# Performance work log

Measured on AMD Instinct MI355X. Metric: run time of the kernel, lower is better.

Reference implementation:

```python
import jax, jax.numpy as jnp
import numpy as np
from jax import lax

MEM = 100          # forced by head_h.view(2, 100)
IN_DIM = 300
N_SENT = 512
N_WORD = 64
VOCAB = 128000
N_HEAD = 8
D = 2 * MEM        # 200
WINDOWS = (1, 2, 3, 4, 5, 6, 7)
NF = 10


def setup_inputs() -> dict:
    key = jax.random.key(0)
    ks = jax.random.split(key, 32)
    def rn(i, shp, s=0.05):
        return jax.random.normal(ks[i], shp, jnp.float32) * s
    inp = dict(
        head_tokens=jax.random.randint(ks[0], (N_WORD,), 1, VOCAB),
        body_tokens=jax.random.randint(ks[1], (N_SENT, N_WORD), 1, VOCAB),
        emb=rn(2, (VOCAB, IN_DIM)),
        wih_f=rn(3, (4 * MEM, IN_DIM)), whh_f=rn(4, (4 * MEM, MEM)),
        bih_f=rn(5, (4 * MEM,)), bhh_f=rn(6, (4 * MEM,)),
        wih_b=rn(7, (4 * MEM, IN_DIM)), whh_b=rn(8, (4 * MEM, MEM)),
        bih_b=rn(9, (4 * MEM,)), bhh_b=rn(10, (4 * MEM,)),
        wq=rn(11, (N_HEAD, D, D)), bq=rn(12, (N_HEAD, D)),
        wk=rn(13, (N_HEAD, D, D)), bk=rn(14, (N_HEAD, D)),
        wv=rn(15, (N_HEAD, D, D)), bv=rn(16, (N_HEAD, D)),
        concat_w=rn(17, (D, N_HEAD * D)), concat_b=rn(18, (D,)),
        feat_w=rn(19, (D, N_SENT * D)), feat_b=rn(20, (D,)),
        conv_b=rn(21, (len(WINDOWS), NF)),
    )
    for j, w in enumerate(WINDOWS):
        inp['conv_w%d' % w] = rn(22 + j, (NF, 1, w, D))
    return inp


def _lstm_dir(x, wih, whh, bih, bhh):
    # x: [T, IN_DIM] -> final hidden [MEM]; torch gate order i, f, g, o
    def step(carry, xt):
        h, c = carry
        g = xt @ wih.T + h @ whh.T + bih + bhh
        i, f, gg, o = jnp.split(g, 4)
        c = jax.nn.sigmoid(f) * c + jax.nn.sigmoid(i) * jnp.tanh(gg)
        h = jax.nn.sigmoid(o) * jnp.tanh(c)
        return (h, c), None
    z = jnp.zeros((MEM,), x.dtype)
    (h, _), _ = lax.scan(step, (z, z), x)
    return h


def _bilstm(x, p):
    wih_f, whh_f, bih_f, bhh_f, wih_b, whh_b, bih_b, bhh_b = p
    hf = _lstm_dir(x, wih_f, whh_f, bih_f, bhh_f)
    hb = _lstm_dir(x[::-1], wih_b, whh_b, bih_b, bhh_b)
    return jnp.concatenate([hf, hb])  # [D]


def _forward(head_tokens, body_tokens, emb, lstm_p, wq, bq, wk, bk, wv, bv,
             concat_w, concat_b, feat_w, feat_b, conv_ws, conv_b):
    # headline encoder
    Bi_Head_h = _bilstm(emb[head_tokens], lstm_p)          # [D]
    # per-sentence BiLSTM over the whole (padded) doc, batched via vmap
    body_x = emb[body_tokens]                              # [S, W, IN_DIM]
    sent_enc = jax.vmap(lambda x: _bilstm(x, lstm_p))(body_x)  # [S, D]
    # 8 single-head self-attentions (indicator == 1 path)
    Q = jnp.einsum('sd,hed->hse', sent_enc, wq) + bq[:, None, :]
    K = jnp.einsum('sd,hed->hse', sent_enc, wk) + bk[:, None, :]
    V = jnp.einsum('sd,hed->hse', sent_enc, wv) + bv[:, None, :]
    sim = jnp.einsum('hse,hte->hst', Q, K) / jnp.sqrt(jnp.float32(D))
    attn = jax.nn.softmax(sim, axis=1)   # torch softmax(dim=0) over [S, S]
    out = jnp.einsum('hst,hte->hse', attn, V)              # [H, S, D]
    head_concat = jnp.transpose(out, (1, 0, 2)).reshape(N_SENT, N_HEAD * D)
    multi = head_concat @ concat_w.T + concat_b            # [S, D]
    high_sent_feature = feat_w @ multi.reshape(-1) + feat_b  # [D]
    # TextCNN over sentence encodings
    x4 = sent_enc[None, None]                              # [1, 1, S, D]
    pooled = []
    for j, (w, cw) in enumerate(zip(WINDOWS, conv_ws)):
        y = lax.conv_general_dilated(
            x4, cw, (1, 1), [(w - 1, w - 1), (0, 0)],
            dimension_numbers=('NCHW', 'OIHW', 'NCHW'))    # [1, NF, S+w-1, 1]
        pooled.append(jnp.max(y[0, :, :, 0], axis=1) + conv_b[j])  # [NF]
    high_sim_pooled = jnp.stack(pooled)                    # [7, NF]
    return high_sent_feature, Bi_Head_h, high_sim_pooled


def reference(head_tokens, body_tokens, emb,
              wih_f, whh_f, bih_f, bhh_f, wih_b, whh_b, bih_b, bhh_b,
              wq, bq, wk, bk, wv, bv, concat_w, concat_b, feat_w, feat_b,
              conv_w1, conv_w2, conv_w3, conv_w4, conv_w5, conv_w6, conv_w7,
              conv_b):
    lstm_p = (wih_f, whh_f, bih_f, bhh_f, wih_b, whh_b, bih_b, bhh_b)
    conv_ws = (conv_w1, conv_w2, conv_w3, conv_w4, conv_w5, conv_w6, conv_w7)
    return _forward(head_tokens, body_tokens, emb, lstm_p, wq, bq, wk, bk,
                    wv, bv, concat_w, concat_b, feat_w, feat_b, conv_ws, conv_b)
```

## Files before the change

kernel.cpp:

```cpp
#include <hip/hip_runtime.h>

typedef _Float16 half8 __attribute__((ext_vector_type(8)));

__device__ __forceinline__ unsigned short f2bf(float f) {
  unsigned u = __float_as_uint(f);
  u += 0x7FFFu + ((u >> 16) & 1u);
  return (unsigned short)(u >> 16);
}
__device__ __forceinline__ float bf2f(unsigned short b) {
  return __uint_as_float(((unsigned)b) << 16);
}
__device__ __forceinline__ float sigf(float x) {
  return __builtin_amdgcn_rcpf(1.f + __expf(-x));
}
__device__ __forceinline__ float tanhf_(float x) {
  float t = __expf(2.f * x);
  return 1.f - 2.f * __builtin_amdgcn_rcpf(t + 1.f);
}

#define NROWS 32832

__global__ __launch_bounds__(256)
void k0_cw4(const float* __restrict__ cw, float* __restrict__ cw4) {
  int idx = blockIdx.x * 256 + threadIdx.x;
  if (idx < 320000) {
    int d = idx / 1600, k = idx % 1600;
    cw4[(size_t)(k >> 2) * 800 + d * 4 + (k & 3)] = cw[idx];
  }
}

__global__ __launch_bounds__(128)
void k1_proj(const int* __restrict__ head_toks, const int* __restrict__ body_toks,
             const float* __restrict__ emb,
             const float* __restrict__ wihf, const float* __restrict__ wihb,
             const float* __restrict__ bihf, const float* __restrict__ bhhf,
             const float* __restrict__ bihb, const float* __restrict__ bhhb,
             unsigned short* __restrict__ XP) {
  __shared__ float At[32][132];
  __shared__ float Wt[32][132];
  __shared__ int toks[128];
  const int tid = threadIdx.x;
  const int r0 = blockIdx.x * 128;
  const int c0 = blockIdx.y * 128;
  if (tid < 128) {
    int r = r0 + tid;
    int tok = 0;
    if (r < NROWS) {
      int u = r >> 6, t = r & 63;
      tok = (u < 512) ? body_toks[u * 64 + t] : head_toks[t];
    }
    toks[tid] = tok;
  }
  const int ty = tid >> 3;
  const int tx = tid & 7;
  float acc[8][16];
#pragma unroll
  for (int i = 0; i < 8; ++i)
#pragma unroll
    for (int j = 0; j < 16; ++j) acc[i][j] = 0.f;

  for (int k0 = 0; k0 < 300; k0 += 32) {
    __syncthreads();
#pragma unroll
    for (int it = 0; it < 8; ++it) {
      int slot = tid + it * 128;
      int rr = slot >> 3, kq = slot & 7;
      int k = k0 + kq * 4;
      float4 v = make_float4(0.f, 0.f, 0.f, 0.f);
      if (k < 300) v = *(const float4*)(emb + (size_t)toks[rr] * 300 + k);
      At[kq * 4 + 0][rr] = v.x; At[kq * 4 + 1][rr] = v.y;
      At[kq * 4 + 2][rr] = v.z; At[kq * 4 + 3][rr] = v.w;
    }
#pragma unroll
    for (int it = 0; it < 8; ++it) {
      int slot = tid + it * 128;
      int cc = slot >> 3, kq = slot & 7;
      int gc = c0 + cc;
      int k = k0 + kq * 4;
      float4 v = make_float4(0.f, 0.f, 0.f, 0.f);
      if (k < 300 && gc < 800) {
        const float* wp = (gc < 400) ? (wihf + (size_t)gc * 300)
                                     : (wihb + (size_t)(gc - 400) * 300);
        v = *(const float4*)(wp + k);
      }
      Wt[kq * 4 + 0][cc] = v.x; Wt[kq * 4 + 1][cc] = v.y;
      Wt[kq * 4 + 2][cc] = v.z; Wt[kq * 4 + 3][cc] = v.w;
    }
    __syncthreads();
#pragma unroll 4
    for (int k = 0; k < 32; ++k) {
      float a[8], b[16];
      *(float4*)&a[0] = *(const float4*)&At[k][ty * 8];
      *(float4*)&a[4] = *(const float4*)&At[k][ty * 8 + 4];
#pragma unroll
      for (int q = 0; q < 4; ++q)
        *(float4*)&b[q * 4] = *(const float4*)&Wt[k][tx * 4 + q * 32];
#pragma unroll
      for (int i = 0; i < 8; ++i)
#pragma unroll
        for (int j = 0; j < 16; ++j)
          acc[i][j] = fmaf(a[i], b[j], acc[i][j]);
    }
  }
  float biasv[16];
#pragma unroll
  for (int j = 0; j < 16; ++j) {
    int gc = c0 + tx * 4 + (j >> 2) * 32 + (j & 3);
    float bv = 0.f;
    if (gc < 400) bv = bihf[gc] + bhhf[gc];
    else if (gc < 800) bv = bihb[gc - 400] + bhhb[gc - 400];
    biasv[j] = bv;
  }
#pragma unroll
  for (int i = 0; i < 8; ++i) {
    int r = r0 + ty * 8 + i;
    if (r >= NROWS) continue;
#pragma unroll
    for (int q = 0; q < 4; ++q) {
      int colq = c0 + tx * 4 + q * 32;
      if (colq >= 800) continue;
      ushort4 pk;
      pk.x = f2bf(acc[i][q * 4 + 0] + biasv[q * 4 + 0]);
      pk.y = f2bf(acc[i][q * 4 + 1] + biasv[q * 4 + 1]);
      pk.z = f2bf(acc[i][q * 4 + 2] + biasv[q * 4 + 2]);
      pk.w = f2bf(acc[i][q * 4 + 3] + biasv[q * 4 + 3]);
      *(ushort4*)(XP + (size_t)r * 800 + colq) = pk;
    }
  }
}

#define K2_W2_SLOTS (4 * 2 * 13 * 64)
#define K2_LDS_BYTES (K2_W2_SLOTS * 16 + 5 * 104 * 4)

__global__ __launch_bounds__(320)
void k2_lstm(const unsigned short* __restrict__ XP,
             const float* __restrict__ whhf, const float* __restrict__ whhb,
             float* __restrict__ sentRM, float* __restrict__ sentT,
             float* __restrict__ dout) {
  extern __shared__ char smem[];
  _Float16* W2 = (_Float16*)smem;
  float* hall = (float*)(smem + K2_W2_SLOTS * 16);
  const int tid = threadIdx.x;
  const int wave = tid >> 6;
  const int lane = tid & 63;
  const int wg = blockIdx.x;
  const bool fwd = wg < 128;
  const int wg2 = fwd ? wg : wg - 128;
  const float* whh = fwd ? whhf : whhb;

  for (int idx = tid; idx < K2_W2_SLOTS; idx += 320) {
    int lane_s = idx & 63;
    int kb = (idx >> 6) % 13;
    int gm = idx / (13 * 64);
    int m = (gm & 1) * 64 + lane_s;
    int g = gm >> 1;
    half8 hv;
#pragma unroll
    for (int i = 0; i < 8; ++i) {
      int k = kb * 8 + i;
      float v = 0.f;
      if (m < 100 && k < 100) v = whh[(size_t)(g * 100 + m) * 100 + k];
      hv[i] = (_Float16)v;
    }
    *(half8*)(W2 + (size_t)idx * 8) = hv;
  }

  int u;
  if (wave < 4) u = wg2 * 4 + wave;
  else u = (wg2 == 0) ? 512 : -1;

  float* hme = hall + wave * 104;
  if (u >= 0) {
    for (int i = lane; i < 104; i += 64) hme[i] = 0.f;
  }
  __syncthreads();
  if (u < 0) return;

  const int off = fwd ? 0 : 400;
  const int doff = fwd ? 0 : 100;
  const int ubase = u * 64;
  const int mm0 = lane;
  const bool v1 = (64 + lane) < 100;
  const int mm1 = v1 ? 64 + lane : 0;

  unsigned short xp[4][2];
  {
    int r = ubase + (fwd ? 0 : 63);
    const unsigned short* rp = XP + (size_t)r * 800 + off;
#pragma unroll
    for (int g = 0; g < 4; ++g) { xp[g][0] = rp[g * 100 + mm0]; xp[g][1] = rp[g * 100 + mm1]; }
  }
  float c0 = 0.f, c1 = 0.f, hl0 = 0.f, hl1 = 0.f;

  for (int t = 0; t < 64; ++t) {
    float acc[4][2];
#pragma unroll
    for (int g = 0; g < 4; ++g) { acc[g][0] = bf2f(xp[g][0]); acc[g][1] = bf2f(xp[g][1]); }
    {
      int tn = (t + 1 < 64) ? t + 1 : 63;
      int r = ubase + (fwd ? tn : 63 - tn);
      const unsigned short* rp = XP + (size_t)r * 800 + off;
#pragma unroll
      for (int g = 0; g < 4; ++g) { xp[g][0] = rp[g * 100 + mm0]; xp[g][1] = rp[g * 100 + mm1]; }
    }
#pragma unroll
    for (int kb = 0; kb < 13; ++kb) {
      float hv[8];
      *(float4*)&hv[0] = *(const float4*)(hme + kb * 8);
      *(float4*)&hv[4] = *(const float4*)(hme + kb * 8 + 4);
#pragma unroll
      for (int g = 0; g < 4; ++g)
#pragma unroll
        for (int ms = 0; ms < 2; ++ms) {
          half8 w = *(const half8*)(W2 + ((size_t)((g * 2 + ms) * 13 + kb) * 64 + lane) * 8);
          float a = acc[g][ms];
#pragma unroll
          for (int i = 0; i < 8; ++i) a = fmaf((float)w[i], hv[i], a);
          acc[g][ms] = a;
        }
    }
    {
      float si = sigf(acc[0][0]), sf = sigf(acc[1][0]), so = sigf(acc[3][0]);
      float tg = tanhf_(acc[2][0]);
      c0 = sf * c0 + si * tg;
      hl0 = so * tanhf_(c0);
      hme[mm0] = hl0;
    }
    if (v1) {
      float si = sigf(acc[0][1]), sf = sigf(acc[1][1]), so = sigf(acc[3][1]);
      float tg = tanhf_(acc[2][1]);
      c1 = sf * c1 + si * tg;
      hl1 = so * tanhf_(c1);
      hme[64 + lane] = hl1;
    }
  }
  {
    int d = doff + mm0;
    sentRM[(size_t)u * 200 + d] = hl0;
    sentT[(size_t)d * 520 + u] = hl0;
    if (u == 512) dout[200 + d] = hl0;
  }
  if (v1) {
    int d = doff + 64 + lane;
    sentRM[(size_t)u * 200 + d] = hl1;
    sentT[(size_t)d * 520 + u] = hl1;
    if (u == 512) dout[200 + d] = hl1;
  }
}

__global__ __launch_bounds__(256)
void k3_qkv(const float* __restrict__ sentT,
            const float* __restrict__ wq, const float* __restrict__ bq,
            const float* __restrict__ wk, const float* __restrict__ bk,
            const float* __restrict__ wv, const float* __restrict__ bv,
            float* __restrict__ QT, float* __restrict__ KT, float* __restrict__ V) {
  __shared__ float slds[32 * 64];
  __shared__ float wt[32 * 204];
  const int tid = threadIdx.x;
  const int mat = blockIdx.x;
  const int h = blockIdx.y;
  const int s0 = blockIdx.z * 64;
  const float* W = (mat == 0) ? wq : (mat == 1) ? wk : wv;
  const float* B = (mat == 0) ? bq : (mat == 1) ? bk : bv;
  W += (size_t)h * 40000;
  B += h * 200;
  const int ts = (tid < 200) ? tid / 25 : 0;
  const int te = (tid < 200) ? tid % 25 : 0;
  float acc[8][8];
#pragma unroll
  for (int i = 0; i < 8; ++i)
#pragma unroll
    for (int j = 0; j < 8; ++j) acc[i][j] = 0.f;

  for (int d0 = 0; d0 < 200; d0 += 32) {
    __syncthreads();
#pragma unroll
    for (int it = 0; it < 8; ++it) {
      int idx = tid + it * 256;
      int dd = idx >> 6, sl = idx & 63;
      int d = d0 + dd;
      slds[idx] = (d < 200) ? sentT[(size_t)d * 520 + s0 + sl] : 0.f;
    }
    for (int idx = tid; idx < 1600; idx += 256) {
      int dq = idx / 200, e = idx % 200;
      int d = d0 + dq * 4;
      float4 v = make_float4(0.f, 0.f, 0.f, 0.f);
      if (d < 200) v = *(const float4*)(W + (size_t)e * 200 + d);
      wt[(dq * 4 + 0) * 204 + e] = v.x; wt[(dq * 4 + 1) * 204 + e] = v.y;
      wt[(dq * 4 + 2) * 204 + e] = v.z; wt[(dq * 4 + 3) * 204 + e] = v.w;
    }
    __syncthreads();
    if (tid < 200) {
#pragma unroll 4
      for (int dd = 0; dd < 32; ++dd) {
        float a[8], b[8];
        *(float4*)&a[0] = *(const float4*)&slds[dd * 64 + ts * 8];
        *(float4*)&a[4] = *(const float4*)&slds[dd * 64 + ts * 8 + 4];
        *(float4*)&b[0] = *(const float4*)&wt[dd * 204 + te * 8];
        *(float4*)&b[4] = *(const float4*)&wt[dd * 204 + te * 8 + 4];
#pragma unroll
        for (int i = 0; i < 8; ++i)
#pragma unroll
          for (int j = 0; j < 8; ++j) acc[i][j] = fmaf(a[i], b[j], acc[i][j]);
      }
    }
  }
  if (tid < 200) {
    if (mat < 2) {
      float* O = (mat == 0) ? QT : KT;
#pragma unroll
      for (int j = 0; j < 8; ++j) {
        int e = te * 8 + j;
        float bb = B[e];
        float vals[8];
#pragma unroll
        for (int i = 0; i < 8; ++i) vals[i] = acc[i][j] + bb;
        float* p = O + (size_t)h * 102400 + (size_t)e * 512 + s0 + ts * 8;
        *(float4*)&p[0] = *(float4*)&vals[0];
        *(float4*)&p[4] = *(float4*)&vals[4];
      }
    } else {
#pragma unroll
      for (int i = 0; i < 8; ++i) {
        float vals[8];
#pragma unroll
        for (int j = 0; j < 8; ++j) vals[j] = acc[i][j] + B[te * 8 + j];
        float* p = V + (size_t)h * 102400 + (size_t)(s0 + ts * 8 + i) * 200 + te * 8;
        *(float4*)&p[0] = *(float4*)&vals[0];
        *(float4*)&p[4] = *(float4*)&vals[4];
      }
    }
  }
}

__global__ __launch_bounds__(128)
void k4_sim(const float* __restrict__ QT, const float* __restrict__ KT,
            float* __restrict__ SIMT) {
  __shared__ float kt[32 * 64];
  __shared__ float qt[32 * 64];
  const int tid = threadIdx.x;
  const int s0 = blockIdx.x * 64;
  const int t0 = blockIdx.y * 64;
  const int h = blockIdx.z;
  const int tt = tid & 15, ss = tid >> 4;
  float acc[4][8];
#pragma unroll
  for (int i = 0; i < 4; ++i)
#pragma unroll
    for (int j = 0; j < 8; ++j) acc[i][j] = 0.f;
  for (int e0 = 0; e0 < 200; e0 += 32) {
    __syncthreads();
#pragma unroll
    for (int it = 0; it < 16; ++it) {
      int idx = tid + it * 128;
      int ee = idx >> 6, tl = idx & 63;
      int e = e0 + ee;
      kt[idx] = (e < 200) ? KT[(size_t)h * 102400 + (size_t)e * 512 + t0 + tl] : 0.f;
      qt[idx] = (e < 200) ? QT[(size_t)h * 102400 + (size_t)e * 512 + s0 + tl] : 0.f;
    }
    __syncthreads();
#pragma unroll 4
    for (int ee = 0; ee < 32; ++ee) {
      float a[4], b[8];
      *(float4*)&a[0] = *(const float4*)&kt[ee * 64 + tt * 4];
      *(float4*)&b[0] = *(const float4*)&qt[ee * 64 + ss * 8];
      *(float4*)&b[4] = *(const float4*)&qt[ee * 64 + ss * 8 + 4];
#pragma unroll
      for (int i = 0; i < 4; ++i)
#pragma unroll
        for (int j = 0; j < 8; ++j) acc[i][j] = fmaf(a[i], b[j], acc[i][j]);
    }
  }
#pragma unroll
  for (int i = 0; i < 4; ++i) {
    float* p = SIMT + ((size_t)h * 512 + t0 + tt * 4 + i) * 512 + s0 + ss * 8;
    *(float4*)&p[0] = *(float4*)&acc[i][0];
    *(float4*)&p[4] = *(float4*)&acc[i][4];
  }
}

__global__ __launch_bounds__(256)
void k5_softmax(float* __restrict__ SIMT) {
  const int tid = threadIdx.x;
  const int row = blockIdx.x * 4 + (tid >> 6);
  const int lane = tid & 63;
  float* p = SIMT + (size_t)row * 512 + lane * 8;
  float4 a = *(float4*)p, b = *(float4*)(p + 4);
  const float sc = 0.07071067811865475f;
  float v[8] = {a.x, a.y, a.z, a.w, b.x, b.y, b.z, b.w};
#pragma unroll
  for (int i = 0; i < 8; ++i) v[i] *= sc;
  float m = v[0];
#pragma unroll
  for (int i = 1; i < 8; ++i) m = fmaxf(m, v[i]);
  for (int d = 1; d < 64; d <<= 1) m = fmaxf(m, __shfl_xor(m, d, 64));
  float sum = 0.f;
#pragma unroll
  for (int i = 0; i < 8; ++i) { v[i] = __expf(v[i] - m); sum += v[i]; }
  for (int d = 1; d < 64; d <<= 1) sum += __shfl_xor(sum, d, 64);
  float inv = __builtin_amdgcn_rcpf(sum);
  a = make_float4(v[0] * inv, v[1] * inv, v[2] * inv, v[3] * inv);
  b = make_float4(v[4] * inv, v[5] * inv, v[6] * inv, v[7] * inv);
  *(float4*)p = a;
  *(float4*)(p + 4) = b;
}

__global__ __launch_bounds__(256)
void k6_av(const float* __restrict__ ATT, const float* __restrict__ V,
           float* __restrict__ OUTb) {
  __shared__ float attl[64 * 36];
  __shared__ float vl[64 * 204];
  const int tid = threadIdx.x;
  const int s0 = blockIdx.x * 32;
  const int h = blockIdx.y;
  const int ts = (tid < 200) ? tid / 25 : 0;
  const int te = (tid < 200) ? tid % 25 : 0;
  float acc[4][8];
#pragma unroll
  for (int i = 0; i < 4; ++i)
#pragma unroll
    for (int j = 0; j < 8; ++j) acc[i][j] = 0.f;
  for (int t0 = 0; t0 < 512; t0 += 64) {
    __syncthreads();
#pragma unroll
    for (int it = 0; it < 8; ++it) {
      int idx = tid + it * 256;
      int tl = idx >> 5, sl = idx & 31;
      attl[tl * 36 + sl] = ATT[((size_t)h * 512 + t0 + tl) * 512 + s0 + sl];
    }
    for (int idx = tid; idx < 12800; idx += 256) {
      int tl = idx / 200, e = idx % 200;
      vl[tl * 204 + e] = V[(size_t)h * 102400 + (size_t)(t0 + tl) * 200 + e];
    }
    __syncthreads();
    if (tid < 200) {
#pragma unroll 2
      for (int tl = 0; tl < 64; ++tl) {
        float a[4], b[8];
        *(float4*)&a[0] = *(const float4*)&attl[tl * 36 + ts * 4];
        *(float4*)&b[0] = *(const float4*)&vl[tl * 204 + te * 8];
        *(float4*)&b[4] = *(const float4*)&vl[tl * 204 + te * 8 + 4];
#pragma unroll
        for (int i = 0; i < 4; ++i)
#pragma unroll
          for (int j = 0; j < 8; ++j) acc[i][j] = fmaf(a[i], b[j], acc[i][j]);
      }
    }
  }
  if (tid < 200) {
#pragma unroll
    for (int i = 0; i < 4; ++i) {
      float* p = OUTb + (size_t)h * 102400 + (size_t)(s0 + ts * 4 + i) * 200 + te * 8;
      *(float4*)&p[0] = *(float4*)&acc[i][0];
      *(float4*)&p[4] = *(float4*)&acc[i][4];
    }
  }
}

__global__ __launch_bounds__(256)
void k7_multi(const float* __restrict__ OUTb, const float* __restrict__ cw4,
              const float* __restrict__ concat_b, float* __restrict__ multi) {
  __shared__ float hc[1600];
  const int tid = threadIdx.x;
  const int s = blockIdx.x;
  for (int idx = tid; idx < 1600; idx += 256) {
    int h = idx / 200, e = idx % 200;
    hc[idx] = OUTb[(size_t)h * 102400 + (size_t)s * 200 + e];
  }
  __syncthreads();
  if (tid < 200) {
    float a = concat_b[tid];
    const float4* cp = (const float4*)cw4 + tid;
    const float4* hp = (const float4*)hc;
    for (int k4 = 0; k4 < 400; ++k4) {
      float4 w = cp[(size_t)k4 * 200];
      float4 x = hp[k4];
      a = fmaf(w.x, x.x, a); a = fmaf(w.y, x.y, a);
      a = fmaf(w.z, x.z, a); a = fmaf(w.w, x.w, a);
    }
    multi[(size_t)s * 200 + tid] = a;
  }
}

__global__ __launch_bounds__(256)
void k8_feat(const float* __restrict__ feat_w, const float* __restrict__ feat_b,
             const float* __restrict__ multi, float* __restrict__ dout) {
  __shared__ float red[4];
  const int tid = threadIdx.x;
  const int d = blockIdx.x;
  const float4* fw = (const float4*)(feat_w + (size_t)d * 102400);
  const float4* mf = (const float4*)multi;
  float a = 0.f;
  for (int i = tid; i < 25600; i += 256) {
    float4 w = fw[i], x = mf[i];
    a = fmaf(w.x, x.x, a); a = fmaf(w.y, x.y, a);
    a = fmaf(w.z, x.z, a); a = fmaf(w.w, x.w, a);
  }
  for (int m_ = 1; m_ < 64; m_ <<= 1) a += __shfl_xor(a, m_, 64);
  if ((tid & 63) == 0) red[tid >> 6] = a;
  __syncthreads();
  if (tid == 0) dout[d] = red[0] + red[1] + red[2] + red[3] + feat_b[d];
}

struct ConvPtrs { const float* p[7]; };

__global__ __launch_bounds__(256)
void k9_conv(ConvPtrs cp, const float* __restrict__ conv_b,
             const float* __restrict__ sent, float* __restrict__ dout) {
  __shared__ float cwl[7 * 200];
  __shared__ float wmax[4];
  const int tid = threadIdx.x;
  const int wi = blockIdx.x;
  const int f = blockIdx.y;
  const int w = wi + 1;
  const float* cw = cp.p[wi] + (size_t)f * w * 200;
  for (int idx = tid; idx < w * 200; idx += 256) cwl[idx] = cw[idx];
  __syncthreads();
  const int wave = tid >> 6, lane = tid & 63;
  float best = -3.4e38f;
  for (int jj = wave; jj < 512 + w - 1; jj += 4) {
    float part = 0.f;
    for (int k = 0; k < w; ++k) {
      int r = jj + k - (w - 1);
      if (r >= 0 && r < 512) {
        const float* sr = sent + (size_t)r * 200;
        const float* cr = cwl + k * 200;
        for (int d = lane; d < 200; d += 64) part = fmaf(cr[d], sr[d], part);
      }
    }
    for (int m_ = 1; m_ < 64; m_ <<= 1) part += __shfl_xor(part, m_, 64);
    best = fmaxf(best, part);
  }
  if (lane == 0) wmax[wave] = best;
  __syncthreads();
  if (tid == 0) {
    float m = fmaxf(fmaxf(wmax[0], wmax[1]), fmaxf(wmax[2], wmax[3]));
    dout[400 + wi * 10 + f] = m + conv_b[wi * 10 + f];
  }
}

extern "C" void kernel_launch(void* const* d_in, const int* in_sizes, int n_in,
                              void* d_out, int out_size, void* d_ws, size_t ws_size,
                              hipStream_t stream) {
  (void)in_sizes; (void)n_in; (void)out_size; (void)ws_size;
  const int*   head_toks = (const int*)d_in[0];
  const int*   body_toks = (const int*)d_in[1];
  const float* emb      = (const float*)d_in[2];
  const float* wih_f    = (const float*)d_in[3];
  const float* whh_f    = (const float*)d_in[4];
  const float* bih_f    = (const float*)d_in[5];
  const float* bhh_f    = (const float*)d_in[6];
  const float* wih_b    = (const float*)d_in[7];
  const float* whh_b    = (const float*)d_in[8];
  const float* bih_b    = (const float*)d_in[9];
  const float* bhh_b    = (const float*)d_in[10];
  const float* wq       = (const float*)d_in[11];
  const float* bq       = (const float*)d_in[12];
  const float* wk       = (const float*)d_in[13];
  const float* bk       = (const float*)d_in[14];
  const float* wv       = (const float*)d_in[15];
  const float* bv       = (const float*)d_in[16];
  const float* concat_w = (const float*)d_in[17];
  const float* concat_b = (const float*)d_in[18];
  const float* feat_w   = (const float*)d_in[19];
  const float* feat_b   = (const float*)d_in[20];
  const float* conv_b   = (const float*)d_in[21];
  float* out = (float*)d_out;
  char* ws = (char*)d_ws;

  size_t off = 0;
  auto take = [&](size_t b) { size_t o = off; off += (b + 255) & ~(size_t)255; return o; };
  unsigned short* XP = (unsigned short*)(ws + take(32832UL * 800 * 2));
  float* sentRM = (float*)(ws + take(513UL * 200 * 4));
  float* sentT  = (float*)(ws + take(200UL * 520 * 4));
  float* QT     = (float*)(ws + take(8UL * 200 * 512 * 4));
  float* KT     = (float*)(ws + take(8UL * 200 * 512 * 4));
  float* Vb     = (float*)(ws + take(8UL * 512 * 200 * 4));
  float* SIMT   = (float*)(ws + take(8UL * 512 * 512 * 4));
  float* OUTb   = (float*)(ws + take(8UL * 512 * 200 * 4));
  float* multi  = (float*)(ws + take(512UL * 200 * 4));
  float* cw4    = (float*)(ws + take(1600UL * 200 * 4));

  k0_cw4<<<1250, 256, 0, stream>>>(concat_w, cw4);
  k1_proj<<<dim3(257, 7), 128, 0, stream>>>(head_toks, body_toks, emb,
                                            wih_f, wih_b, bih_f, bhh_f, bih_b, bhh_b, XP);
  static bool attr_set = []() {
    hipFuncSetAttribute(reinterpret_cast<const void*>(k2_lstm),
                        hipFuncAttributeMaxDynamicSharedMemorySize, 160 * 1024);
    return true;
  }();
  (void)attr_set;
  k2_lstm<<<256, 320, K2_LDS_BYTES, stream>>>(XP, whh_f, whh_b, sentRM, sentT, out);
  k3_qkv<<<dim3(3, 8, 8), 256, 0, stream>>>(sentT, wq, bq, wk, bk, wv, bv, QT, KT, Vb);
  k4_sim<<<dim3(8, 8, 8), 128, 0, stream>>>(QT, KT, SIMT);
  k5_softmax<<<1024, 256, 0, stream>>>(SIMT);
  k6_av<<<dim3(16, 8), 256, 0, stream>>>(SIMT, Vb, OUTb);
  k7_multi<<<512, 256, 0, stream>>>(OUTb, cw4, concat_b, multi);
  k8_feat<<<200, 256, 0, stream>>>(feat_w, feat_b, multi, out);
  ConvPtrs cps;
  for (int i = 0; i < 7; ++i) cps.p[i] = (const float*)d_in[22 + i];
  k9_conv<<<dim3(7, 10), 256, 0, stream>>>(cps, conv_b, sentRM, out);
}
```

Before: 1.478 ms.

## Rewrite LSTM recurrence with MFMA over 16 sequences per block and interleaved gates

The recurrent LSTM kernel now processes 16 sequences per workgroup, computing h·Whh with 16x16x32 fp16 MFMA instructions. The recurrent weights stay in registers as MFMA fragments and h is kept in swizzled LDS. The input projection is stored as fp16 with gate columns interleaved per hidden unit, so each lane reads its i/f/g/o inputs as one half4, double-buffered into LDS. The concat projection kernel also handles 8 sentences per block to reuse weight loads. This trades many scalar-FMA workgroups for far fewer MFMA-based ones (66 blocks), lowers grid parallelism, and changes precision (fp16 instead of bf16 for XP, fp16 h).

```diff
diff --git a/kernel.cpp b/kernel.cpp
--- a/kernel.cpp
+++ b/kernel.cpp
@@ -1,15 +1,9 @@
 #include <hip/hip_runtime.h>
 
 typedef _Float16 half8 __attribute__((ext_vector_type(8)));
-
-__device__ __forceinline__ unsigned short f2bf(float f) {
-  unsigned u = __float_as_uint(f);
-  u += 0x7FFFu + ((u >> 16) & 1u);
-  return (unsigned short)(u >> 16);
-}
-__device__ __forceinline__ float bf2f(unsigned short b) {
-  return __uint_as_float(((unsigned)b) << 16);
-}
+typedef _Float16 half4 __attribute__((ext_vector_type(4)));
+typedef float f32x4 __attribute__((ext_vector_type(4)));
+
 __device__ __forceinline__ float sigf(float x) {
   return __builtin_amdgcn_rcpf(1.f + __expf(-x));
 }
@@ -35,7 +29,7 @@
              const float* __restrict__ wihf, const float* __restrict__ wihb,
              const float* __restrict__ bihf, const float* __restrict__ bhhf,
              const float* __restrict__ bihb, const float* __restrict__ bhhb,
-             unsigned short* __restrict__ XP) {
+             _Float16* __restrict__ XP) {
   __shared__ float At[32][132];
   __shared__ float Wt[32][132];
   __shared__ int toks[128];
@@ -79,8 +73,11 @@
       int k = k0 + kq * 4;
       float4 v = make_float4(0.f, 0.f, 0.f, 0.f);
       if (k < 300 && gc < 800) {
-        const float* wp = (gc < 400) ? (wihf + (size_t)gc * 300)
-                                     : (wihb + (size_t)(gc - 400) * 300);
+        int dir = gc >= 400;
+        int rem = gc - dir * 400;
+        int orow = (rem & 3) * 100 + (rem >> 2);
+        const float* wp = dir ? (wihb + (size_t)orow * 300)
+                              : (wihf + (size_t)orow * 300);
         v = *(const float4*)(wp + k);
       }
       Wt[kq * 4 + 0][cc] = v.x; Wt[kq * 4 + 1][cc] = v.y;
@@ -107,8 +104,12 @@
   for (int j = 0; j < 16; ++j) {
     int gc = c0 + tx * 4 + (j >> 2) * 32 + (j & 3);
     float bv = 0.f;
-    if (gc < 400) bv = bihf[gc] + bhhf[gc];
-    else if (gc < 800) bv = bihb[gc - 400] + bhhb[gc - 400];
+    if (gc < 800) {
+      int dir = gc >= 400;
+      int rem = gc - dir * 400;
+      int orow = (rem & 3) * 100 + (rem >> 2);
+      bv = dir ? (bihb[orow] + bhhb[orow]) : (bihf[orow] + bhhf[orow]);
+    }
     biasv[j] = bv;
   }
 #pragma unroll
@@ -119,132 +120,140 @@
     for (int q = 0; q < 4; ++q) {
       int colq = c0 + tx * 4 + q * 32;
       if (colq >= 800) continue;
-      ushort4 pk;
-      pk.x = f2bf(acc[i][q * 4 + 0] + biasv[q * 4 + 0]);
-      pk.y = f2bf(acc[i][q * 4 + 1] + biasv[q * 4 + 1]);
-      pk.z = f2bf(acc[i][q * 4 + 2] + biasv[q * 4 + 2]);
-      pk.w = f2bf(acc[i][q * 4 + 3] + biasv[q * 4 + 3]);
-      *(ushort4*)(XP + (size_t)r * 800 + colq) = pk;
-    }
-  }
-}
-
-#define K2_W2_SLOTS (4 * 2 * 13 * 64)
-#define K2_LDS_BYTES (K2_W2_SLOTS * 16 + 5 * 104 * 4)
-
-__global__ __launch_bounds__(320)
-void k2_lstm(const unsigned short* __restrict__ XP,
+      half4 pk;
+      pk[0] = (_Float16)(acc[i][q * 4 + 0] + biasv[q * 4 + 0]);
+      pk[1] = (_Float16)(acc[i][q * 4 + 1] + biasv[q * 4 + 1]);
+      pk[2] = (_Float16)(acc[i][q * 4 + 2] + biasv[q * 4 + 2]);
+      pk[3] = (_Float16)(acc[i][q * 4 + 3] + biasv[q * 4 + 3]);
+      *(half4*)(XP + (size_t)r * 800 + colq) = pk;
+    }
+  }
+}
+
+#define XPL_ROW 1616
+#define XPL_BUF (16 * XPL_ROW)
+#define K2_LDS (4096 + 2 * XPL_BUF)
+
+__global__ __launch_bounds__(256, 1)
+void k2_lstm(const _Float16* __restrict__ XP,
              const float* __restrict__ whhf, const float* __restrict__ whhb,
              float* __restrict__ sentRM, float* __restrict__ sentT,
              float* __restrict__ dout) {
-  extern __shared__ char smem[];
-  _Float16* W2 = (_Float16*)smem;
-  float* hall = (float*)(smem + K2_W2_SLOTS * 16);
-  const int tid = threadIdx.x;
-  const int wave = tid >> 6;
-  const int lane = tid & 63;
-  const int wg = blockIdx.x;
-  const bool fwd = wg < 128;
-  const int wg2 = fwd ? wg : wg - 128;
+  __shared__ char smem[K2_LDS];
+  _Float16* H = (_Float16*)smem;
+  char* XPL = smem + 4096;
+  const int tid = threadIdx.x;
+  const int w = tid >> 6;
+  const int l = tid & 63;
+  const int b = blockIdx.x;
+  const bool fwd = b < 33;
+  const int bb = fwd ? b : b - 33;
   const float* whh = fwd ? whhf : whhb;
-
-  for (int idx = tid; idx < K2_W2_SLOTS; idx += 320) {
-    int lane_s = idx & 63;
-    int kb = (idx >> 6) % 13;
-    int gm = idx / (13 * 64);
-    int m = (gm & 1) * 64 + lane_s;
-    int g = gm >> 1;
-    half8 hv;
-#pragma unroll
-    for (int i = 0; i < 8; ++i) {
-      int k = kb * 8 + i;
-      float v = 0.f;
-      if (m < 100 && k < 100) v = whh[(size_t)(g * 100 + m) * 100 + k];
-      hv[i] = (_Float16)v;
-    }
-    *(half8*)(W2 + (size_t)idx * 8) = hv;
-  }
-
-  int u;
-  if (wave < 4) u = wg2 * 4 + wave;
-  else u = (wg2 == 0) ? 512 : -1;
-
-  float* hme = hall + wave * 104;
-  if (u >= 0) {
-    for (int i = lane; i < 104; i += 64) hme[i] = 0.f;
-  }
+  const int seq0 = bb * 16;
+  const int xoff = fwd ? 0 : 400;
+  const int doff = fwd ? 0 : 100;
+  const int u = l & 15;
+  const int kq = l >> 4;
+
+  half8 afrag[7][4];
+#pragma unroll
+  for (int mtl = 0; mtl < 7; ++mtl) {
+    int gr = (w * 7 + mtl) * 16 + u;
+    int m = gr >> 2, g = gr & 3;
+#pragma unroll
+    for (int kt = 0; kt < 4; ++kt) {
+      half8 v;
+#pragma unroll
+      for (int i = 0; i < 8; ++i) {
+        int kk = kt * 32 + kq * 8 + i;
+        float x = (m < 100 && kk < 100) ? whh[(size_t)(g * 100 + m) * 100 + kk] : 0.f;
+        v[i] = (_Float16)x;
+      }
+      afrag[mtl][kt] = v;
+    }
+  }
+
+  for (int i = tid; i < 2048; i += 256) H[i] = (_Float16)0.f;
+
+  auto stage = [&](int t, int buf) {
+    int tidx = fwd ? t : 63 - t;
+#pragma unroll
+    for (int it = 0; it < 7; ++it) {
+      int idx = it * 64 + l;
+      if (idx < 400) {
+        int ul = 4 * w + idx / 100;
+        int ch = idx % 100;
+        int seq = seq0 + ul; if (seq > 512) seq = 512;
+        half8 v = *(const half8*)(XP + ((size_t)seq * 64 + tidx) * 800 + ch * 8);
+        *(half8*)(XPL + buf * XPL_BUF + ul * XPL_ROW + ch * 16) = v;
+      }
+    }
+  };
+  stage(0, 0);
   __syncthreads();
-  if (u < 0) return;
-
-  const int off = fwd ? 0 : 400;
-  const int doff = fwd ? 0 : 100;
-  const int ubase = u * 64;
-  const int mm0 = lane;
-  const bool v1 = (64 + lane) < 100;
-  const int mm1 = v1 ? 64 + lane : 0;
-
-  unsigned short xp[4][2];
-  {
-    int r = ubase + (fwd ? 0 : 63);
-    const unsigned short* rp = XP + (size_t)r * 800 + off;
-#pragma unroll
-    for (int g = 0; g < 4; ++g) { xp[g][0] = rp[g * 100 + mm0]; xp[g][1] = rp[g * 100 + mm1]; }
-  }
-  float c0 = 0.f, c1 = 0.f, hl0 = 0.f, hl1 = 0.f;
+
+  float cst[7], hst[7];
+#pragma unroll
+  for (int i = 0; i < 7; ++i) { cst[i] = 0.f; hst[i] = 0.f; }
+
+  const int hswz = (u & 7) << 4;
 
   for (int t = 0; t < 64; ++t) {
-    float acc[4][2];
-#pragma unroll
-    for (int g = 0; g < 4; ++g) { acc[g][0] = bf2f(xp[g][0]); acc[g][1] = bf2f(xp[g][1]); }
-    {
-      int tn = (t + 1 < 64) ? t + 1 : 63;
-      int r = ubase + (fwd ? tn : 63 - tn);
-      const unsigned short* rp = XP + (size_t)r * 800 + off;
-#pragma unroll
-      for (int g = 0; g < 4; ++g) { xp[g][0] = rp[g * 100 + mm0]; xp[g][1] = rp[g * 100 + mm1]; }
-    }
-#pragma unroll
-    for (int kb = 0; kb < 13; ++kb) {
-      float hv[8];
-      *(float4*)&hv[0] = *(const float4*)(hme + kb * 8);
-      *(float4*)&hv[4] = *(const float4*)(hme + kb * 8 + 4);
-#pragma unroll
-      for (int g = 0; g < 4; ++g)
-#pragma unroll
-        for (int ms = 0; ms < 2; ++ms) {
-          half8 w = *(const half8*)(W2 + ((size_t)((g * 2 + ms) * 13 + kb) * 64 + lane) * 8);
-          float a = acc[g][ms];
-#pragma unroll
-          for (int i = 0; i < 8; ++i) a = fmaf((float)w[i], hv[i], a);
-          acc[g][ms] = a;
-        }
-    }
-    {
-      float si = sigf(acc[0][0]), sf = sigf(acc[1][0]), so = sigf(acc[3][0]);
-      float tg = tanhf_(acc[2][0]);
-      c0 = sf * c0 + si * tg;
-      hl0 = so * tanhf_(c0);
-      hme[mm0] = hl0;
-    }
-    if (v1) {
-      float si = sigf(acc[0][1]), sf = sigf(acc[1][1]), so = sigf(acc[3][1]);
-      float tg = tanhf_(acc[2][1]);
-      c1 = sf * c1 + si * tg;
-      hl1 = so * tanhf_(c1);
-      hme[64 + lane] = hl1;
-    }
-  }
-  {
-    int d = doff + mm0;
-    sentRM[(size_t)u * 200 + d] = hl0;
-    sentT[(size_t)d * 520 + u] = hl0;
-    if (u == 512) dout[200 + d] = hl0;
-  }
-  if (v1) {
-    int d = doff + 64 + lane;
-    sentRM[(size_t)u * 200 + d] = hl1;
-    sentT[(size_t)d * 520 + u] = hl1;
-    if (u == 512) dout[200 + d] = hl1;
+    const int buf = t & 1;
+    if (t + 1 < 64) stage(t + 1, buf ^ 1);
+
+    half8 bfrag[4];
+#pragma unroll
+    for (int kt = 0; kt < 4; ++kt) {
+      int byte = u * 256 + ((kt * 64 + kq * 16) ^ hswz);
+      bfrag[kt] = *(const half8*)((char*)H + byte);
+    }
+    f32x4 c[7];
+#pragma unroll
+    for (int mtl = 0; mtl < 7; ++mtl) {
+      f32x4 acc = {0.f, 0.f, 0.f, 0.f};
+#pragma unroll
+      for (int kt = 0; kt < 4; ++kt)
+        acc = __builtin_amdgcn_mfma_f32_16x16x32_f16(afrag[mtl][kt], bfrag[kt], acc, 0, 0, 0);
+      c[mtl] = acc;
+    }
+    __syncthreads();
+
+#pragma unroll
+    for (int mtl = 0; mtl < 7; ++mtl) {
+      int m = (w * 7 + mtl) * 4 + kq;
+      if (m < 100) {
+        half4 xp = *(const half4*)(XPL + buf * XPL_BUF + u * XPL_ROW + (xoff + m * 4) * 2);
+        float pi = c[mtl][0] + (float)xp[0];
+        float pf = c[mtl][1] + (float)xp[1];
+        float pg = c[mtl][2] + (float)xp[2];
+        float po = c[mtl][3] + (float)xp[3];
+        float i_ = sigf(pi), f_ = sigf(pf), o_ = sigf(po);
+        float g_ = tanhf_(pg);
+        float cc = f_ * cst[mtl] + i_ * g_;
+        cst[mtl] = cc;
+        float h = o_ * tanhf_(cc);
+        hst[mtl] = h;
+        int byte = u * 256 + ((m * 2) ^ hswz);
+        *(_Float16*)((char*)H + byte) = (_Float16)h;
+      }
+    }
+    __syncthreads();
+  }
+
+  const int seq = seq0 + u;
+  if (seq <= 512) {
+#pragma unroll
+    for (int mtl = 0; mtl < 7; ++mtl) {
+      int m = (w * 7 + mtl) * 4 + kq;
+      if (m < 100) {
+        int d = doff + m;
+        float h = hst[mtl];
+        sentRM[(size_t)seq * 200 + d] = h;
+        sentT[(size_t)d * 520 + seq] = h;
+        if (seq == 512) dout[200 + d] = h;
+      }
+    }
   }
 }
 
@@ -460,25 +469,32 @@
 __global__ __launch_bounds__(256)
 void k7_multi(const float* __restrict__ OUTb, const float* __restrict__ cw4,
               const float* __restrict__ concat_b, float* __restrict__ multi) {
-  __shared__ float hc[1600];
-  const int tid = threadIdx.x;
-  const int s = blockIdx.x;
-  for (int idx = tid; idx < 1600; idx += 256) {
-    int h = idx / 200, e = idx % 200;
-    hc[idx] = OUTb[(size_t)h * 102400 + (size_t)s * 200 + e];
+  __shared__ float hc[8][1600];
+  const int tid = threadIdx.x;
+  const int s0 = blockIdx.x * 8;
+  for (int idx = tid; idx < 12800; idx += 256) {
+    int sl = idx / 1600, k = idx % 1600;
+    int h = k / 200, e = k % 200;
+    hc[sl][k] = OUTb[(size_t)h * 102400 + (size_t)(s0 + sl) * 200 + e];
   }
   __syncthreads();
   if (tid < 200) {
-    float a = concat_b[tid];
+    float acc[8];
+    float bb = concat_b[tid];
+#pragma unroll
+    for (int s = 0; s < 8; ++s) acc[s] = bb;
     const float4* cp = (const float4*)cw4 + tid;
-    const float4* hp = (const float4*)hc;
     for (int k4 = 0; k4 < 400; ++k4) {
-      float4 w = cp[(size_t)k4 * 200];
-      float4 x = hp[k4];
-      a = fmaf(w.x, x.x, a); a = fmaf(w.y, x.y, a);
-      a = fmaf(w.z, x.z, a); a = fmaf(w.w, x.w, a);
-    }
-    multi[(size_t)s * 200 + tid] = a;
+      float4 wv = cp[(size_t)k4 * 200];
+#pragma unroll
+      for (int s = 0; s < 8; ++s) {
+        float4 x = *(const float4*)&hc[s][k4 * 4];
+        acc[s] = fmaf(wv.x, x.x, acc[s]); acc[s] = fmaf(wv.y, x.y, acc[s]);
+        acc[s] = fmaf(wv.z, x.z, acc[s]); acc[s] = fmaf(wv.w, x.w, acc[s]);
+      }
+    }
+#pragma unroll
+    for (int s = 0; s < 8; ++s) multi[(size_t)(s0 + s) * 200 + tid] = acc[s];
   }
 }
 
@@ -570,7 +586,7 @@
 
   size_t off = 0;
   auto take = [&](size_t b) { size_t o = off; off += (b + 255) & ~(size_t)255; return o; };
-  unsigned short* XP = (unsigned short*)(ws + take(32832UL * 800 * 2));
+  _Float16* XP  = (_Float16*)(ws + take(32832UL * 800 * 2));
   float* sentRM = (float*)(ws + take(513UL * 200 * 4));
   float* sentT  = (float*)(ws + take(200UL * 520 * 4));
   float* QT     = (float*)(ws + take(8UL * 200 * 512 * 4));
@@ -584,18 +600,12 @@
   k0_cw4<<<1250, 256, 0, stream>>>(concat_w, cw4);
   k1_proj<<<dim3(257, 7), 128, 0, stream>>>(head_toks, body_toks, emb,
                                             wih_f, wih_b, bih_f, bhh_f, bih_b, bhh_b, XP);
-  static bool attr_set = []() {
-    hipFuncSetAttribute(reinterpret_cast<const void*>(k2_lstm),
-                        hipFuncAttributeMaxDynamicSharedMemorySize, 160 * 1024);
-    return true;
-  }();
-  (void)attr_set;
-  k2_lstm<<<256, 320, K2_LDS_BYTES, stream>>>(XP, whh_f, whh_b, sentRM, sentT, out);
+  k2_lstm<<<66, 256, 0, stream>>>(XP, whh_f, whh_b, sentRM, sentT, out);
   k3_qkv<<<dim3(3, 8, 8), 256, 0, stream>>>(sentT, wq, bq, wk, bk, wv, bv, QT, KT, Vb);
   k4_sim<<<dim3(8, 8, 8), 128, 0, stream>>>(QT, KT, SIMT);
   k5_softmax<<<1024, 256, 0, stream>>>(SIMT);
   k6_av<<<dim3(16, 8), 256, 0, stream>>>(SIMT, Vb, OUTb);
-  k7_multi<<<512, 256, 0, stream>>>(OUTb, cw4, concat_b, multi);
+  k7_multi<<<64, 256, 0, stream>>>(OUTb, cw4, concat_b, multi);
   k8_feat<<<200, 256, 0, stream>>>(feat_w, feat_b, multi, out);
   ConvPtrs cps;
   for (int i = 0; i < 7; ++i) cps.p[i] = (const float*)d_in[22 + i];
```

After: 1.401 ms. 5.2% less time.
